# Kernel tuning notes

Measured on AMD Instinct MI355X. Metric: run time of the kernel, lower is better.

## Reference

```python
import jax, jax.numpy as jnp
import numpy as np

B, T, D = 8, 2048, 256
EPS_NORM = 1e-8
EPS_LN = 1e-6


def _layer_norm(x, gamma, beta):
    mu = jnp.mean(x, axis=-1, keepdims=True)
    var = jnp.var(x, axis=-1, keepdims=True)
    return (x - mu) * jax.lax.rsqrt(var + EPS_LN) * gamma + beta


def setup_inputs() -> dict:
    key = jax.random.key(0)
    ks = jax.random.split(key, 8)
    xav = np.sqrt(2.0 / (D + D)).astype(np.float32)  # xavier_uniform-ish scale
    a_fea = jax.random.normal(ks[0], (B, T, D), jnp.float32)
    v_fea = jax.random.normal(ks[1], (B, T, D), jnp.float32)
    Wv1 = jax.random.normal(ks[2], (D, D), jnp.float32) * xav
    Wv2 = jax.random.normal(ks[3], (D, D), jnp.float32) * xav
    Wa1 = jax.random.normal(ks[4], (D, D), jnp.float32) * xav
    Wa2 = jax.random.normal(ks[5], (D, D), jnp.float32) * xav
    ln_gamma = jnp.ones((D,), jnp.float32)
    ln_beta = jnp.zeros((D,), jnp.float32)
    thr_val = jnp.asarray(0.099, jnp.float32)
    return {"a_fea": a_fea, "v_fea": v_fea, "Wv1": Wv1, "Wv2": Wv2,
            "Wa1": Wa1, "Wa2": Wa2, "ln_gamma": ln_gamma, "ln_beta": ln_beta,
            "thr_val": thr_val}


def reference(a_fea, v_fea, Wv1, Wv2, Wa1, Wa2, ln_gamma, ln_beta, thr_val):
    # Dropout is identity in eval mode. Linear(bias=False): x @ W^T; here W is [in, out].
    v_b1 = jax.nn.relu(jnp.einsum('btd,dh->bth', v_fea, Wv1))
    v_b2 = jax.nn.relu(jnp.einsum('btd,dh->bth', v_fea, Wv2))
    a_b1 = jax.nn.relu(jnp.einsum('btd,dh->bth', a_fea, Wa1))
    a_b2 = jax.nn.relu(jnp.einsum('btd,dh->bth', a_fea, Wa2))

    scale = 1.0 / jnp.sqrt(jnp.asarray(v_b2.shape[2], jnp.float32))
    # relu-gated cross-modal scores [B, Tv, Ta]
    beta = jax.nn.relu(jnp.einsum('bvh,bah->bva', v_b2, a_b1) * scale)

    # v->a: normalize over audio axis, threshold-sparsify
    beta_va = beta / (jnp.sum(beta, axis=-1, keepdims=True) + EPS_NORM)
    gamma_va = jnp.where(beta_va > thr_val, beta_va, 0.0)
    # a->v: transpose of UN-normalized beta (faithful to source ordering)
    beta_av = jnp.swapaxes(beta, 1, 2)
    beta_av = beta_av / (jnp.sum(beta_av, axis=-1, keepdims=True) + EPS_NORM)
    gamma_av = jnp.where(beta_av > thr_val, beta_av, 0.0)

    a_pos = jnp.einsum('bva,bah->bvh', gamma_va, a_b2)
    v_pos = jnp.einsum('bav,bvh->bah', gamma_av, v_b1)

    v_psp = _layer_norm(v_fea + a_pos, ln_gamma, ln_beta)
    a_psp = _layer_norm(a_fea + v_pos, ln_gamma, ln_beta)
    return (v_psp + a_psp) * 0.5
```

## Files before the change

### kernel.cpp

```cpp
#include <hip/hip_runtime.h>
#include <stdint.h>

#define B_ 8
#define T_ 2048
#define D_ 256
#define M_ (B_*T_)

typedef uint16_t u16;
typedef __attribute__((ext_vector_type(8))) short   short8;
typedef __attribute__((ext_vector_type(8))) __bf16  bf16x8;
typedef __attribute__((ext_vector_type(4))) float   f32x4;
typedef __attribute__((ext_vector_type(4))) uint32_t u32x4;

__device__ __forceinline__ float bf2f(u16 b){
    union { uint32_t u; float f; } v; v.u = ((uint32_t)b) << 16; return v.f;
}
__device__ __forceinline__ u16 f2bf(float f){
    union { float f; uint32_t u; } v; v.f = f;
    uint32_t u = v.u;
    u += 0x7FFFu + ((u >> 16) & 1u);
    return (u16)(u >> 16);
}

typedef __attribute__((address_space(1))) void gvoid;
typedef __attribute__((address_space(3))) void lvoid;
typedef __attribute__((address_space(3))) const u16 lds_cu16;
__device__ __forceinline__ void gl16(const void* g, void* l){
    __builtin_amdgcn_global_load_lds((gvoid*)(unsigned long long)g, (lvoid*)l, 16, 0, 0);
}

__global__ void k_detect(const uint32_t* g, int* flag){
    *flag = (g[0] == 0x3F803F80u) ? 0 : 1;
}

struct WtArgs { const void* w[4]; u16* wt[4]; const int* flag; };

__global__ __launch_bounds__(256) void k_wt(WtArgs a){
    int f32in = *a.flag;
    int m = blockIdx.y;
    int d = blockIdx.x;
    int h = threadIdx.x;
    float val;
    if (f32in) val = ((const float*)a.w[m])[(size_t)d * D_ + h];
    else       val = bf2f(((const u16*)a.w[m])[(size_t)d * D_ + h]);
    a.wt[m][(size_t)h * D_ + d] = f2bf(val);
}

struct ProjArgs { const void* x[4]; const u16* wt[4]; u16* y[4]; u16* yt[4]; const int* flag; };

__global__ __launch_bounds__(256) void k_proj(ProjArgs args){
    __shared__ __align__(16) u16 Xs[128][72];
    __shared__ __align__(16) u16 Ws[128][72];
    int f32in = *args.flag;
    int id = blockIdx.x;
    int m  = id & 127;
    int vh = id >> 7;
    int hh = vh & 1;
    int v  = vh >> 1;
    const u16* Wt = args.wt[v];
    u16*       Y  = args.y[v];
    u16*       YT = args.yt[v];
    int t_base = m * 128;
    int h_base = hh * 128;

    int tid  = threadIdx.x;
    int w    = tid >> 6, lane = tid & 63;
    int wm   = w >> 1, wn = w & 1;
    int l15  = lane & 15, quad = lane >> 4;

    int srow = tid >> 1;
    int shalf = tid & 1;

    f32x4 acc[4][4];
#pragma unroll
    for (int i = 0; i < 4; ++i)
#pragma unroll
        for (int j = 0; j < 4; ++j) acc[i][j] = (f32x4){0.f,0.f,0.f,0.f};

    float4 pXf[8];
    short8 pXb[4];
    short8 pW[4];

    const float* Xf = (const float*)args.x[v] + (size_t)(t_base + srow)*D_ + shalf*32;
    const u16*   Xb = (const u16*)args.x[v]   + (size_t)(t_base + srow)*D_ + shalf*32;
    const u16*   Wp = Wt + (size_t)(h_base + srow)*D_ + shalf*32;

    if (f32in){
#pragma unroll
        for (int i = 0; i < 8; ++i) pXf[i] = *(const float4*)(Xf + i*4);
    } else {
#pragma unroll
        for (int i = 0; i < 4; ++i) pXb[i] = *(const short8*)(Xb + i*8);
    }
#pragma unroll
    for (int i = 0; i < 4; ++i) pW[i] = *(const short8*)(Wp + i*8);

    for (int k0 = 0; k0 < D_; k0 += 64){
        __syncthreads();
        if (f32in){
#pragma unroll
            for (int i = 0; i < 4; ++i){
                float4 a0 = pXf[i*2], a1 = pXf[i*2+1];
                short8 o;
                o[0]=(short)f2bf(a0.x); o[1]=(short)f2bf(a0.y); o[2]=(short)f2bf(a0.z); o[3]=(short)f2bf(a0.w);
                o[4]=(short)f2bf(a1.x); o[5]=(short)f2bf(a1.y); o[6]=(short)f2bf(a1.z); o[7]=(short)f2bf(a1.w);
                *(short8*)(&Xs[srow][shalf*32 + i*8]) = o;
            }
        } else {
#pragma unroll
            for (int i = 0; i < 4; ++i) *(short8*)(&Xs[srow][shalf*32 + i*8]) = pXb[i];
        }
#pragma unroll
        for (int i = 0; i < 4; ++i) *(short8*)(&Ws[srow][shalf*32 + i*8]) = pW[i];

        int kn = k0 + 64;
        if (kn < D_){
            if (f32in){
#pragma unroll
                for (int i = 0; i < 8; ++i) pXf[i] = *(const float4*)(Xf + kn + i*4);
            } else {
#pragma unroll
                for (int i = 0; i < 4; ++i) pXb[i] = *(const short8*)(Xb + kn + i*8);
            }
#pragma unroll
            for (int i = 0; i < 4; ++i) pW[i] = *(const short8*)(Wp + kn + i*8);
        }
        __syncthreads();

#pragma unroll
        for (int kc = 0; kc < 2; ++kc){
            bf16x8 af[4], bf[4];
#pragma unroll
            for (int i = 0; i < 4; ++i){
                af[i] = __builtin_bit_cast(bf16x8,
                         *(const short8*)(&Xs[wm*64 + i*16 + l15][kc*32 + quad*8]));
                bf[i] = __builtin_bit_cast(bf16x8,
                         *(const short8*)(&Ws[wn*64 + i*16 + l15][kc*32 + quad*8]));
            }
#pragma unroll
            for (int mt = 0; mt < 4; ++mt)
#pragma unroll
                for (int nt = 0; nt < 4; ++nt)
                    acc[mt][nt] = __builtin_amdgcn_mfma_f32_16x16x32_bf16(
                                      af[mt], bf[nt], acc[mt][nt], 0, 0, 0);
        }
    }

    int v0 = t_base + wm*64;
    int h0 = h_base + wn*64;
#pragma unroll
    for (int mt = 0; mt < 4; ++mt){
#pragma unroll
        for (int nt = 0; nt < 4; ++nt){
            int col = h0 + nt*16 + l15;
            u16 q[4];
#pragma unroll
            for (int r = 0; r < 4; ++r){
                float s = acc[mt][nt][r]; s = s > 0.f ? s : 0.f;
                q[r] = f2bf(s);
            }
            if (Y){
#pragma unroll
                for (int r = 0; r < 4; ++r)
                    Y[(size_t)(v0 + mt*16 + quad*4 + r)*D_ + col] = q[r];
            }
            if (YT){
                int row0 = v0 + mt*16 + quad*4;
                int bb   = row0 >> 11;
                int tl   = row0 & (T_-1);
                uint2 pk;
                pk.x = (uint32_t)q[0] | ((uint32_t)q[1] << 16);
                pk.y = (uint32_t)q[2] | ((uint32_t)q[3] << 16);
                *(uint2*)(YT + ((size_t)(bb*D_ + col))*T_ + tl) = pk;
            }
        }
    }
}

__global__ __launch_bounds__(256) void k_score(const u16* vb2, const u16* ab1,
                                               u16* beta_t,
                                               float* rowsum, float* colsum){
    __shared__ __align__(16) u16 As[128][72];
    __shared__ __align__(16) u16 Bs[128][72];
    int id = blockIdx.x;
    int b  = id & 7;
    int t  = id >> 3;
    int mb = t & 15;
    int ab = t >> 4;
    int tid  = threadIdx.x;
    int w    = tid >> 6, lane = tid & 63;
    int wm   = w >> 1, wn = w & 1;
    int l15  = lane & 15, quad = lane >> 4;
    int v_base = mb*128;
    int a_base = ab*128;

    const u16* vb = vb2 + (size_t)b*T_*D_;
    const u16* an = ab1 + (size_t)b*T_*D_;
    u16* tb = beta_t + (((size_t)b*16 + mb)*16 + ab)*16384;
    float* rs  = rowsum + b*T_;
    float* cs  = colsum + b*T_;

    int kk = tid & 7;
    int mm = tid >> 3;

    f32x4 acc[4][4];
#pragma unroll
    for (int i = 0; i < 4; ++i)
#pragma unroll
        for (int j = 0; j < 4; ++j) acc[i][j] = (f32x4){0.f,0.f,0.f,0.f};

    short8 pA[4], pB[4];
#pragma unroll
    for (int i = 0; i < 4; ++i){
        int row = mm + i*32;
        pA[i] = *(const short8*)(vb + (size_t)(v_base + row)*D_ + kk*8);
        pB[i] = *(const short8*)(an + (size_t)(a_base + row)*D_ + kk*8);
    }

    for (int k0 = 0; k0 < D_; k0 += 64){
        __syncthreads();
#pragma unroll
        for (int i = 0; i < 4; ++i){
            int row = mm + i*32;
            *(short8*)(&As[row][kk*8]) = pA[i];
            *(short8*)(&Bs[row][kk*8]) = pB[i];
        }
        int kn = k0 + 64;
        if (kn < D_){
#pragma unroll
            for (int i = 0; i < 4; ++i){
                int row = mm + i*32;
                pA[i] = *(const short8*)(vb + (size_t)(v_base + row)*D_ + kn + kk*8);
                pB[i] = *(const short8*)(an + (size_t)(a_base + row)*D_ + kn + kk*8);
            }
        }
        __syncthreads();

#pragma unroll
        for (int kc = 0; kc < 2; ++kc){
            bf16x8 af[4], bf[4];
#pragma unroll
            for (int i = 0; i < 4; ++i){
                af[i] = __builtin_bit_cast(bf16x8,
                         *(const short8*)(&As[wm*64 + i*16 + l15][kc*32 + quad*8]));
                bf[i] = __builtin_bit_cast(bf16x8,
                         *(const short8*)(&Bs[wn*64 + i*16 + l15][kc*32 + quad*8]));
            }
#pragma unroll
            for (int mt = 0; mt < 4; ++mt)
#pragma unroll
                for (int nt = 0; nt < 4; ++nt)
                    acc[mt][nt] = __builtin_amdgcn_mfma_f32_16x16x32_bf16(
                                      af[mt], bf[nt], acc[mt][nt], 0, 0, 0);
        }
    }

    float rsum[4][4];
    float csum[4] = {0.f,0.f,0.f,0.f};
#pragma unroll
    for (int mt = 0; mt < 4; ++mt)
#pragma unroll
        for (int r = 0; r < 4; ++r) rsum[mt][r] = 0.f;

#pragma unroll
    for (int mt = 0; mt < 4; ++mt){
#pragma unroll
        for (int nt = 0; nt < 4; ++nt){
            int aa = wn*64 + nt*16 + l15;
#pragma unroll
            for (int r = 0; r < 4; ++r){
                float s = acc[mt][nt][r] * 0.0625f;
                s = s > 0.f ? s : 0.f;
                tb[(size_t)(wm*64 + mt*16 + quad*4 + r)*128 + aa] = f2bf(s);
                rsum[mt][r] += s;
                csum[nt]    += s;
            }
        }
    }
    int v0 = v_base + wm*64;
    int a0 = a_base + wn*64;
#pragma unroll
    for (int mt = 0; mt < 4; ++mt){
#pragma unroll
        for (int r = 0; r < 4; ++r){
            float v = rsum[mt][r];
            v += __shfl_xor(v, 1);
            v += __shfl_xor(v, 2);
            v += __shfl_xor(v, 4);
            v += __shfl_xor(v, 8);
            if (l15 == 0) atomicAdd(&rs[v0 + mt*16 + quad*4 + r], v);
        }
    }
#pragma unroll
    for (int nt = 0; nt < 4; ++nt){
        float v = csum[nt];
        v += __shfl_xor(v, 16);
        v += __shfl_xor(v, 32);
        if (quad == 0) atomicAdd(&cs[a0 + nt*16 + l15], v);
    }
}

__global__ __launch_bounds__(256) void k_pos7(const u16* beta_t,
                                              const u16* ab2T, const u16* vb1T,
                                              const float* rowsum, const float* colsum,
                                              const void* thrp, const int* flag,
                                              u16* apos, u16* vpos){
    __shared__ __align__(16) u16 SL[2][2][128*64];
    int f32in = *flag;
    int s  = blockIdx.x;
    int id = (s & 7) * 64 + (s >> 3);
    int nb    = id & 1;
    int mb    = (id >> 1) & 15;
    int b     = (id >> 5) & 7;
    int which = id >> 8;

    const u16* TB  = beta_t + (size_t)b*16*16*16384;
    const u16* Bt  = (which ? vb1T  : ab2T) + (size_t)b*T_*D_;
    const float* nrm = (which ? colsum : rowsum) + b*T_;
    u16* outb = (which ? vpos : apos) + (size_t)b*T_*D_;

    float thr = f32in ? *(const float*)thrp : bf2f(*(const u16*)thrp);

    int tid = threadIdx.x;
    int w = tid >> 6, lane = tid & 63;
    int l15 = lane & 15, quad = lane >> 4;

    int m0 = mb * 128;
    int h0 = nb * 128;

    int schk = (lane & 7) ^ ((lane >> 3) & 7);
    const u16* gB = Bt + (size_t)(h0 + w*32 + (lane >> 3))*T_ + schk*8;

    int vl = ((lane >> 3) & 3)*8 + ((lane >> 5) & 1)*4 + ((lane >> 1) & 3);
    int ha = lane & 1;

    uint32_t thp[2];
#pragma unroll
    for (int i = 0; i < 2; ++i){
        float ts = thr * (nrm[m0 + w*32 + i*16 + l15] + 1e-8f);
        union { float f; uint32_t u; } cv; cv.f = ts;
        uint32_t th16 = cv.u >> 16;
        thp[i] = th16 * 0x10001u;
    }

    f32x4 acc[2][8];
#pragma unroll
    for (int i = 0; i < 2; ++i)
#pragma unroll
        for (int j = 0; j < 8; ++j) acc[i][j] = (f32x4){0.f,0.f,0.f,0.f};

    if (which == 0){
#pragma unroll
        for (int c = 0; c < 4; ++c){
            const u16* src = TB + ((size_t)mb*16 + 0)*16384
                           + (size_t)(w*32 + c*8 + (lane>>3))*128 + schk*8;
            gl16(src, &SL[0][0][(w*32 + c*8)*64]);
        }
    } else {
#pragma unroll
        for (int p = 0; p < 4; ++p){
            int sa = w*2 + (p & 1), kc = p >> 1;
            const u16* src = TB + ((size_t)0*16 + mb)*16384
                           + (size_t)(kc*32 + vl)*128 + sa*16 + ha*8;
            gl16(src, (u16*)SL[0][0] + sa*1024 + kc*512);
        }
    }
#pragma unroll
    for (int c = 0; c < 4; ++c)
        gl16(gB + (size_t)c*8*T_, &SL[0][1][(w*32 + c*8)*64]);

    int q = 0;
    for (int k0 = 0; k0 < T_; k0 += 64){
        int kn = k0 + 64;
        __builtin_amdgcn_sched_barrier(0);
        __builtin_amdgcn_s_barrier();
        __builtin_amdgcn_sched_barrier(0);
        if (kn < T_){
            if (which == 0){
                int at = kn >> 7, col0 = kn & 127;
#pragma unroll
                for (int c = 0; c < 4; ++c){
                    const u16* src = TB + ((size_t)mb*16 + at)*16384
                                   + (size_t)(w*32 + c*8 + (lane>>3))*128 + col0 + schk*8;
                    gl16(src, &SL[q^1][0][(w*32 + c*8)*64]);
                }
            } else {
                int vt = kn >> 7, v0 = kn & 127;
#pragma unroll
                for (int p = 0; p < 4; ++p){
                    int sa = w*2 + (p & 1), kc = p >> 1;
                    const u16* src = TB + ((size_t)vt*16 + mb)*16384
                                   + (size_t)(v0 + kc*32 + vl)*128 + sa*16 + ha*8;
                    gl16(src, (u16*)SL[q^1][0] + sa*1024 + kc*512);
                }
            }
#pragma unroll
            for (int c = 0; c < 4; ++c)
                gl16(gB + (size_t)c*8*T_ + kn, &SL[q^1][1][(w*32 + c*8)*64]);
            __builtin_amdgcn_sched_barrier(0);
            asm volatile("s_waitcnt vmcnt(8)" ::: "memory");
        } else {
            asm volatile("s_waitcnt vmcnt(0)" ::: "memory");
        }
        __builtin_amdgcn_sched_barrier(0);
        __builtin_amdgcn_s_barrier();
        __builtin_amdgcn_sched_barrier(0);

        const u16* Asb = &SL[q][0][0];
        const u16* Bsb = &SL[q][1][0];
#pragma unroll
        for (int kc = 0; kc < 2; ++kc){
            int sw = ((kc*4 + quad) ^ (l15 & 7)) * 8;
            bf16x8 af[2];
            if (which == 0){
#pragma unroll
                for (int i = 0; i < 2; ++i){
                    u32x4 ra = *(const u32x4*)(Asb + (size_t)(w*32 + i*16 + l15)*64 + sw);
                    u32x4 om;
#pragma unroll
                    for (int jd = 0; jd < 4; ++jd){
                        uint32_t tt, mm2;
                        asm("v_pk_sub_u16 %0, %1, %2" : "=v"(tt) : "v"(thp[i]), "v"(ra[jd]));
                        asm("v_pk_ashrrev_i16 %0, 15, %1" : "=v"(mm2) : "v"(tt));
                        om[jd] = ra[jd] & mm2;
                    }
                    af[i] = __builtin_bit_cast(bf16x8, om);
                }
            } else {
                uint2 t0[2], t1[2];
#pragma unroll
                for (int i = 0; i < 2; ++i){
                    lds_cu16* pa = (lds_cu16*)(Asb + (w*2 + i)*1024 + kc*512 + lane*4);
                    asm volatile("ds_read_b64_tr_b16 %0, %1"
                                 : "=v"(t0[i]) : "v"(pa) : "memory");
                    asm volatile("ds_read_b64_tr_b16 %0, %1 offset:512"
                                 : "=v"(t1[i]) : "v"(pa) : "memory");
                }
                asm volatile("s_waitcnt lgkmcnt(0)" ::: "memory");
                __builtin_amdgcn_sched_barrier(0);
#pragma unroll
                for (int i = 0; i < 2; ++i){
                    u32x4 ra = {t0[i].x, t0[i].y, t1[i].x, t1[i].y};
                    u32x4 om;
#pragma unroll
                    for (int jd = 0; jd < 4; ++jd){
                        uint32_t tt, mm2;
                        asm("v_pk_sub_u16 %0, %1, %2" : "=v"(tt) : "v"(thp[i]), "v"(ra[jd]));
                        asm("v_pk_ashrrev_i16 %0, 15, %1" : "=v"(mm2) : "v"(tt));
                        om[jd] = ra[jd] & mm2;
                    }
                    af[i] = __builtin_bit_cast(bf16x8, om);
                }
            }
#pragma unroll
            for (int nt = 0; nt < 8; ++nt){
                bf16x8 bfr = __builtin_bit_cast(bf16x8,
                              *(const short8*)(Bsb + (size_t)(nt*16 + l15)*64 + sw));
                acc[0][nt] = __builtin_amdgcn_mfma_f32_16x16x32_bf16(
                                  af[0], bfr, acc[0][nt], 0, 0, 0);
                acc[1][nt] = __builtin_amdgcn_mfma_f32_16x16x32_bf16(
                                  af[1], bfr, acc[1][nt], 0, 0, 0);
            }
        }
        q ^= 1;
    }

#pragma unroll
    for (int i = 0; i < 2; ++i){
#pragma unroll
        for (int r = 0; r < 4; ++r){
            int row = m0 + w*32 + i*16 + quad*4 + r;
            float iv = 1.f / (nrm[row] + 1e-8f);
#pragma unroll
            for (int nt = 0; nt < 8; ++nt)
                outb[(size_t)row*D_ + h0 + nt*16 + l15] =
                    f2bf(acc[i][nt][r] * iv);
        }
    }
}

__global__ __launch_bounds__(256) void k_ln(const void* vfea, const void* afea,
                                            const u16* apos, const u16* vpos,
                                            const void* g, const void* lnb,
                                            const int* flag, void* out){
    int f32in = *flag;
    int row = blockIdx.x;
    int c   = threadIdx.x;
    size_t idx = (size_t)row * D_ + c;
    float xv = f32in ? ((const float*)vfea)[idx] : bf2f(((const u16*)vfea)[idx]);
    float xa = f32in ? ((const float*)afea)[idx] : bf2f(((const u16*)afea)[idx]);
    float x1 = xv + bf2f(apos[idx]);
    float x2 = xa + bf2f(vpos[idx]);
    float s1 = x1, q1 = x1*x1, s2 = x2, q2 = x2*x2;
#pragma unroll
    for (int off = 1; off < 64; off <<= 1){
        s1 += __shfl_xor(s1, off);
        q1 += __shfl_xor(q1, off);
        s2 += __shfl_xor(s2, off);
        q2 += __shfl_xor(q2, off);
    }
    __shared__ float red[4][4];
    int wave = threadIdx.x >> 6;
    if ((threadIdx.x & 63) == 0){
        red[0][wave] = s1; red[1][wave] = q1; red[2][wave] = s2; red[3][wave] = q2;
    }
    __syncthreads();
    s1 = red[0][0]+red[0][1]+red[0][2]+red[0][3];
    q1 = red[1][0]+red[1][1]+red[1][2]+red[1][3];
    s2 = red[2][0]+red[2][1]+red[2][2]+red[2][3];
    q2 = red[3][0]+red[3][1]+red[3][2]+red[3][3];
    const float invD = 1.f / (float)D_;
    float mu1 = s1*invD, mu2 = s2*invD;
    float var1 = q1*invD - mu1*mu1;
    float var2 = q2*invD - mu2*mu2;
    float rs1 = rsqrtf(var1 + 1e-6f);
    float rs2 = rsqrtf(var2 + 1e-6f);
    float gg = f32in ? ((const float*)g)[c]   : bf2f(((const u16*)g)[c]);
    float bv = f32in ? ((const float*)lnb)[c] : bf2f(((const u16*)lnb)[c]);
    float y = 0.5f * (((x1-mu1)*rs1)*gg + bv + ((x2-mu2)*rs2)*gg + bv);
    if (f32in) ((float*)out)[idx] = y;
    else       ((u16*)out)[idx]   = f2bf(y);
}

extern "C" void kernel_launch(void* const* d_in, const int* in_sizes, int n_in,
                              void* d_out, int out_size, void* d_ws, size_t ws_size,
                              hipStream_t stream){
    (void)in_sizes; (void)n_in; (void)out_size; (void)ws_size;
    const void* a_fea = d_in[0];
    const void* v_fea = d_in[1];
    const void* Wv1   = d_in[2];
    const void* Wv2   = d_in[3];
    const void* Wa1   = d_in[4];
    const void* Wa2   = d_in[5];
    const void* lng   = d_in[6];
    const void* lnb   = d_in[7];
    const void* thrp  = d_in[8];
    char* ws = (char*)d_ws;

    const size_t ACT  = (size_t)M_ * D_ * 2;
    const size_t BETA = (size_t)B_ * T_ * T_ * 2;
    size_t off_wt    = 0;
    size_t off_vb2   = 524288;
    size_t off_ab1   = off_vb2  + ACT;
    size_t off_vb1T  = off_ab1  + ACT;
    size_t off_ab2T  = off_vb1T + ACT;
    size_t off_beta  = off_ab2T + ACT;
    size_t off_rsum  = off_beta + BETA;
    size_t off_csum  = off_rsum + (size_t)B_*T_*4;
    size_t off_apos  = off_csum + (size_t)B_*T_*4;
    size_t off_vpos  = off_apos + ACT;
    size_t off_flag  = off_vpos + ACT;

    u16* wt0   = (u16*)(ws + off_wt);
    u16* vb2   = (u16*)(ws + off_vb2);
    u16* ab1   = (u16*)(ws + off_ab1);
    u16* vb1T  = (u16*)(ws + off_vb1T);
    u16* ab2T  = (u16*)(ws + off_ab2T);
    u16* beta  = (u16*)(ws + off_beta);
    float* rowsum = (float*)(ws + off_rsum);
    float* colsum = (float*)(ws + off_csum);
    u16*   apos   = (u16*)(ws + off_apos);
    u16*   vpos   = (u16*)(ws + off_vpos);
    int*   flag   = (int*)(ws + off_flag);

    hipMemsetAsync(ws + off_rsum, 0, 2 * (size_t)B_ * T_ * sizeof(float), stream);

    k_detect<<<1, 1, 0, stream>>>((const uint32_t*)lng, flag);

    WtArgs wa;
    wa.w[0] = Wv1; wa.w[1] = Wv2; wa.w[2] = Wa1; wa.w[3] = Wa2;
    for (int i = 0; i < 4; ++i) wa.wt[i] = wt0 + (size_t)i * D_ * D_;
    wa.flag = flag;
    k_wt<<<dim3(256,4), 256, 0, stream>>>(wa);

    ProjArgs pa;
    pa.x[0] = v_fea; pa.x[1] = v_fea; pa.x[2] = a_fea; pa.x[3] = a_fea;
    for (int i = 0; i < 4; ++i) pa.wt[i] = wa.wt[i];
    pa.y[0] = nullptr; pa.y[1] = vb2; pa.y[2] = ab1; pa.y[3] = nullptr;
    pa.yt[0] = vb1T;   pa.yt[1] = nullptr; pa.yt[2] = nullptr; pa.yt[3] = ab2T;
    pa.flag = flag;
    k_proj<<<4*2*(M_/128), 256, 0, stream>>>(pa);

    k_score<<<8*16*16, 256, 0, stream>>>(vb2, ab1, beta, rowsum, colsum);

    k_pos7<<<512, 256, 0, stream>>>(beta, ab2T, vb1T, rowsum, colsum,
                                    thrp, flag, apos, vpos);

    k_ln<<<M_, 256, 0, stream>>>(v_fea, a_fea, apos, vpos, lng, lnb, flag, d_out);
}
```

Baseline: 225.6 us.

## Fold dtype detect into k_wt, stage score tile via LDS, row-per-wave layernorm

Three separate changes. The dtype-detect kernel is removed: every k_wt thread now reads the gamma word itself and one thread writes the flag, which saves a launch. k_score packs its bf16 beta outputs into registers, transposes them through a padded LDS tile that reuses the operand buffers, and writes 16-byte coalesced rows instead of scattered 2-byte stores. k_ln now handles one row per wave with 4-wide vector loads, which removes the LDS cross-wave reduction and the barrier and cuts the grid to a quarter of its former size.

```diff
diff --git a/kernel.cpp b/kernel.cpp
--- a/kernel.cpp
+++ b/kernel.cpp
@@ -29,14 +29,11 @@
     __builtin_amdgcn_global_load_lds((gvoid*)(unsigned long long)g, (lvoid*)l, 16, 0, 0);
 }
 
-__global__ void k_detect(const uint32_t* g, int* flag){
-    *flag = (g[0] == 0x3F803F80u) ? 0 : 1;
-}
-
-struct WtArgs { const void* w[4]; u16* wt[4]; const int* flag; };
+struct WtArgs { const void* w[4]; u16* wt[4]; const void* lng; int* flag; };
 
 __global__ __launch_bounds__(256) void k_wt(WtArgs a){
-    int f32in = *a.flag;
+    int f32in = (((const uint32_t*)a.lng)[0] == 0x3F803F80u) ? 0 : 1;
+    if (blockIdx.x == 0 && blockIdx.y == 0 && threadIdx.x == 0) *a.flag = f32in;
     int m = blockIdx.y;
     int d = blockIdx.x;
     int h = threadIdx.x;
@@ -180,8 +177,9 @@
 __global__ __launch_bounds__(256) void k_score(const u16* vb2, const u16* ab1,
                                                u16* beta_t,
                                                float* rowsum, float* colsum){
-    __shared__ __align__(16) u16 As[128][72];
-    __shared__ __align__(16) u16 Bs[128][72];
+    __shared__ __align__(16) u16 SMEM[2*128*72];
+    u16 (*As)[72] = (u16(*)[72])(SMEM);
+    u16 (*Bs)[72] = (u16(*)[72])(SMEM + 128*72);
     int id = blockIdx.x;
     int b  = id & 7;
     int t  = id >> 3;
@@ -257,6 +255,7 @@
 
     float rsum[4][4];
     float csum[4] = {0.f,0.f,0.f,0.f};
+    uint2 qq[4][4];
 #pragma unroll
     for (int mt = 0; mt < 4; ++mt)
 #pragma unroll
@@ -266,15 +265,17 @@
     for (int mt = 0; mt < 4; ++mt){
 #pragma unroll
         for (int nt = 0; nt < 4; ++nt){
-            int aa = wn*64 + nt*16 + l15;
+            u16 q[4];
 #pragma unroll
             for (int r = 0; r < 4; ++r){
                 float s = acc[mt][nt][r] * 0.0625f;
                 s = s > 0.f ? s : 0.f;
-                tb[(size_t)(wm*64 + mt*16 + quad*4 + r)*128 + aa] = f2bf(s);
+                q[r] = f2bf(s);
                 rsum[mt][r] += s;
                 csum[nt]    += s;
             }
+            qq[mt][nt].x = (uint32_t)q[0] | ((uint32_t)q[1] << 16);
+            qq[mt][nt].y = (uint32_t)q[2] | ((uint32_t)q[3] << 16);
         }
     }
     int v0 = v_base + wm*64;
@@ -297,6 +298,31 @@
         v += __shfl_xor(v, 16);
         v += __shfl_xor(v, 32);
         if (quad == 0) atomicAdd(&cs[a0 + nt*16 + l15], v);
+    }
+
+    u16* tile = SMEM;
+    __syncthreads();
+#pragma unroll
+    for (int mt = 0; mt < 4; ++mt){
+#pragma unroll
+        for (int nt = 0; nt < 4; ++nt){
+            int aa = wn*64 + nt*16 + l15;
+            uint2 p = qq[mt][nt];
+#pragma unroll
+            for (int r = 0; r < 4; ++r){
+                int va = wm*64 + mt*16 + quad*4 + r;
+                u16 qv = (u16)((r < 2 ? p.x : p.y) >> ((r & 1) * 16));
+                tile[(size_t)va*136 + aa] = qv;
+            }
+        }
+    }
+    __syncthreads();
+#pragma unroll
+    for (int it = 0; it < 8; ++it){
+        int flat = it*256 + tid;
+        int vv = flat >> 4, ch = flat & 15;
+        u32x4 d = *(const u32x4*)(tile + (size_t)vv*136 + ch*8);
+        *(u32x4*)(tb + (size_t)vv*128 + ch*8) = d;
     }
 }
 
@@ -484,14 +510,37 @@
                                             const void* g, const void* lnb,
                                             const int* flag, void* out){
     int f32in = *flag;
-    int row = blockIdx.x;
-    int c   = threadIdx.x;
-    size_t idx = (size_t)row * D_ + c;
-    float xv = f32in ? ((const float*)vfea)[idx] : bf2f(((const u16*)vfea)[idx]);
-    float xa = f32in ? ((const float*)afea)[idx] : bf2f(((const u16*)afea)[idx]);
-    float x1 = xv + bf2f(apos[idx]);
-    float x2 = xa + bf2f(vpos[idx]);
-    float s1 = x1, q1 = x1*x1, s2 = x2, q2 = x2*x2;
+    int wave = threadIdx.x >> 6, lane = threadIdx.x & 63;
+    int row  = blockIdx.x * 4 + wave;
+    int c0   = lane * 4;
+    size_t idx = (size_t)row * D_ + c0;
+
+    float xv[4], xa[4];
+    if (f32in){
+        float4 v4 = *(const float4*)((const float*)vfea + idx);
+        float4 a4 = *(const float4*)((const float*)afea + idx);
+        xv[0]=v4.x; xv[1]=v4.y; xv[2]=v4.z; xv[3]=v4.w;
+        xa[0]=a4.x; xa[1]=a4.y; xa[2]=a4.z; xa[3]=a4.w;
+    } else {
+        ushort4 v4 = *(const ushort4*)((const u16*)vfea + idx);
+        ushort4 a4 = *(const ushort4*)((const u16*)afea + idx);
+        xv[0]=bf2f(v4.x); xv[1]=bf2f(v4.y); xv[2]=bf2f(v4.z); xv[3]=bf2f(v4.w);
+        xa[0]=bf2f(a4.x); xa[1]=bf2f(a4.y); xa[2]=bf2f(a4.z); xa[3]=bf2f(a4.w);
+    }
+    ushort4 ap = *(const ushort4*)(apos + idx);
+    ushort4 vp = *(const ushort4*)(vpos + idx);
+    float x1[4], x2[4];
+    x1[0] = xv[0] + bf2f(ap.x); x1[1] = xv[1] + bf2f(ap.y);
+    x1[2] = xv[2] + bf2f(ap.z); x1[3] = xv[3] + bf2f(ap.w);
+    x2[0] = xa[0] + bf2f(vp.x); x2[1] = xa[1] + bf2f(vp.y);
+    x2[2] = xa[2] + bf2f(vp.z); x2[3] = xa[3] + bf2f(vp.w);
+
+    float s1 = 0.f, q1 = 0.f, s2 = 0.f, q2 = 0.f;
+#pragma unroll
+    for (int e = 0; e < 4; ++e){
+        s1 += x1[e]; q1 += x1[e]*x1[e];
+        s2 += x2[e]; q2 += x2[e]*x2[e];
+    }
 #pragma unroll
     for (int off = 1; off < 64; off <<= 1){
         s1 += __shfl_xor(s1, off);
@@ -499,27 +548,38 @@
         s2 += __shfl_xor(s2, off);
         q2 += __shfl_xor(q2, off);
     }
-    __shared__ float red[4][4];
-    int wave = threadIdx.x >> 6;
-    if ((threadIdx.x & 63) == 0){
-        red[0][wave] = s1; red[1][wave] = q1; red[2][wave] = s2; red[3][wave] = q2;
-    }
-    __syncthreads();
-    s1 = red[0][0]+red[0][1]+red[0][2]+red[0][3];
-    q1 = red[1][0]+red[1][1]+red[1][2]+red[1][3];
-    s2 = red[2][0]+red[2][1]+red[2][2]+red[2][3];
-    q2 = red[3][0]+red[3][1]+red[3][2]+red[3][3];
     const float invD = 1.f / (float)D_;
     float mu1 = s1*invD, mu2 = s2*invD;
     float var1 = q1*invD - mu1*mu1;
     float var2 = q2*invD - mu2*mu2;
     float rs1 = rsqrtf(var1 + 1e-6f);
     float rs2 = rsqrtf(var2 + 1e-6f);
-    float gg = f32in ? ((const float*)g)[c]   : bf2f(((const u16*)g)[c]);
-    float bv = f32in ? ((const float*)lnb)[c] : bf2f(((const u16*)lnb)[c]);
-    float y = 0.5f * (((x1-mu1)*rs1)*gg + bv + ((x2-mu2)*rs2)*gg + bv);
-    if (f32in) ((float*)out)[idx] = y;
-    else       ((u16*)out)[idx]   = f2bf(y);
+
+    float gg[4], bv[4];
+    if (f32in){
+        float4 g4 = *(const float4*)((const float*)g   + c0);
+        float4 b4 = *(const float4*)((const float*)lnb + c0);
+        gg[0]=g4.x; gg[1]=g4.y; gg[2]=g4.z; gg[3]=g4.w;
+        bv[0]=b4.x; bv[1]=b4.y; bv[2]=b4.z; bv[3]=b4.w;
+    } else {
+        ushort4 g4 = *(const ushort4*)((const u16*)g   + c0);
+        ushort4 b4 = *(const ushort4*)((const u16*)lnb + c0);
+        gg[0]=bf2f(g4.x); gg[1]=bf2f(g4.y); gg[2]=bf2f(g4.z); gg[3]=bf2f(g4.w);
+        bv[0]=bf2f(b4.x); bv[1]=bf2f(b4.y); bv[2]=bf2f(b4.z); bv[3]=bf2f(b4.w);
+    }
+    float y[4];
+#pragma unroll
+    for (int e = 0; e < 4; ++e)
+        y[e] = 0.5f * (((x1[e]-mu1)*rs1)*gg[e] + bv[e] + ((x2[e]-mu2)*rs2)*gg[e] + bv[e]);
+
+    if (f32in){
+        float4 o; o.x=y[0]; o.y=y[1]; o.z=y[2]; o.w=y[3];
+        *(float4*)((float*)out + idx) = o;
+    } else {
+        ushort4 o;
+        o.x=f2bf(y[0]); o.y=f2bf(y[1]); o.z=f2bf(y[2]); o.w=f2bf(y[3]);
+        *(ushort4*)((u16*)out + idx) = o;
+    }
 }
 
 extern "C" void kernel_launch(void* const* d_in, const int* in_sizes, int n_in,
@@ -565,12 +625,10 @@
 
     hipMemsetAsync(ws + off_rsum, 0, 2 * (size_t)B_ * T_ * sizeof(float), stream);
 
-    k_detect<<<1, 1, 0, stream>>>((const uint32_t*)lng, flag);
-
     WtArgs wa;
     wa.w[0] = Wv1; wa.w[1] = Wv2; wa.w[2] = Wa1; wa.w[3] = Wa2;
     for (int i = 0; i < 4; ++i) wa.wt[i] = wt0 + (size_t)i * D_ * D_;
-    wa.flag = flag;
+    wa.lng = lng; wa.flag = flag;
     k_wt<<<dim3(256,4), 256, 0, stream>>>(wa);
 
     ProjArgs pa;
@@ -586,5 +644,5 @@
     k_pos7<<<512, 256, 0, stream>>>(beta, ab2T, vb1T, rowsum, colsum,
                                     thrp, flag, apos, vpos);
 
-    k_ln<<<M_, 256, 0, stream>>>(v_fea, a_fea, apos, vpos, lng, lnb, flag, d_out);
-}
+    k_ln<<<M_/4, 256, 0, stream>>>(v_fea, a_fea, apos, vpos, lng, lnb, flag, d_out);
+}
```

Result: faster. 218.9 us, median of 2 (-3.0%).
